# Optimization experiments

Measured on AMD Instinct MI355X. Metric: run time of the kernel, lower is better.

Reference implementation:

```python
import jax, jax.numpy as jnp
import numpy as np
from jax import lax

SCORE_THRESHOLD = 0.01
NMS_THRESHOLD = 0.5
MAX_DETECTIONS = 100
PRE_NMS_TOPK = 512  # fixed-shape candidate pool per class (tf NMS is unbounded; 512 >> max_detections covers it)
NEG_INF = -jnp.inf


def setup_inputs() -> dict:
    key = jax.random.key(0)
    k1, k2, k3, k4, k5 = jax.random.split(key, 5)
    B, N, C = 32, 50000, 10
    # valid (x1,y1,x2,y2) boxes: random top-left + positive width/height
    xy = jax.random.uniform(k1, (B, N, 2), dtype=jnp.float32) * 500.0
    wh = jax.random.uniform(k2, (B, N, 2), dtype=jnp.float32) * 100.0 + 1.0
    boxes = jnp.concatenate([xy, xy + wh], axis=-1)
    classification = jax.random.uniform(k3, (B, N, C), dtype=jnp.float32)
    rotation = jax.random.normal(k4, (B, N, 3), dtype=jnp.float32)
    translation = jax.random.normal(k5, (B, N, 3), dtype=jnp.float32)
    return {"boxes": boxes, "classification": classification,
            "rotation": rotation, "translation": translation}


def _iou_matrix(b):  # b: (K,4) in (x1,y1,x2,y2)
    x1, y1, x2, y2 = b[:, 0], b[:, 1], b[:, 2], b[:, 3]
    area = (x2 - x1) * (y2 - y1)  # (K,)
    ix1 = jnp.maximum(x1[:, None], x1[None, :])
    iy1 = jnp.maximum(y1[:, None], y1[None, :])
    ix2 = jnp.minimum(x2[:, None], x2[None, :])
    iy2 = jnp.minimum(y2[:, None], y2[None, :])
    inter = jnp.maximum(ix2 - ix1, 0.0) * jnp.maximum(iy2 - iy1, 0.0)
    union = area[:, None] + area[None, :] - inter
    return jnp.where(union > 0.0, inter / union, 0.0)  # (K,K)


def _greedy_nms_keep(iou, valid):
    # iou: (K,K) for boxes already sorted by descending score; valid: (K,) bool
    K = iou.shape[0]
    def body(suppressed, xs):
        iou_row, valid_i, i = xs
        keep_i = valid_i & jnp.logical_not(suppressed[i])
        suppressed = jnp.where(keep_i, suppressed | (iou_row > NMS_THRESHOLD), suppressed)
        return suppressed, keep_i
    _, keep = lax.scan(body, jnp.zeros((K,), bool), (iou, valid, jnp.arange(K)))
    return keep


def _per_class(scores, boxes_i):
    # scores: (N,), boxes_i: (N,4) -> kept candidate scores (K,) (-inf where dropped) and anchor idx (K,)
    sc = jnp.where(scores > SCORE_THRESHOLD, scores, NEG_INF)
    vals, idx = lax.top_k(sc, PRE_NMS_TOPK)          # sorted desc
    valid = vals > SCORE_THRESHOLD                    # also false for -inf pads
    iou = _iou_matrix(boxes_i[idx])
    keep = _greedy_nms_keep(iou, valid)
    keep = keep & (jnp.cumsum(keep.astype(jnp.int32)) <= MAX_DETECTIONS)
    return jnp.where(keep, vals, NEG_INF), idx


def _per_image(boxes_i, cls_i, rot_i, trans_i):
    # boxes_i (N,4), cls_i (N,C), rot_i (N,3), trans_i (N,3)
    C = cls_i.shape[1]
    sc_ck, idx_ck = jax.vmap(_per_class, in_axes=(1, None))(cls_i, boxes_i)  # (C,K)
    labels_ck = jnp.broadcast_to(jnp.arange(C, dtype=jnp.int32)[:, None], sc_ck.shape)
    sc_flat = sc_ck.reshape(-1)
    idx_flat = idx_ck.reshape(-1)
    lab_flat = labels_ck.reshape(-1)
    top_scores, sel = lax.top_k(sc_flat, MAX_DETECTIONS)   # global top-k across classes
    sel_idx = idx_flat[sel]
    sel_lab = lab_flat[sel]
    valid = jnp.isfinite(top_scores)
    out_boxes = jnp.where(valid[:, None], boxes_i[sel_idx], -1.0)
    out_scores = jnp.where(valid, top_scores, -1.0)
    out_labels = jnp.where(valid, sel_lab, -1).astype(jnp.int32)
    out_rot = jnp.where(valid[:, None], rot_i[sel_idx], -1.0)
    out_trans = jnp.where(valid[:, None], trans_i[sel_idx], -1.0)
    return out_boxes, out_scores, out_labels, out_rot, out_trans


def reference(boxes, classification, rotation, translation):
    return jax.vmap(_per_image)(boxes, classification, rotation, translation)
```

## Files before the change

kernel.cpp:

```cpp
#include <hip/hip_runtime.h>
#include <math.h>

typedef unsigned int u32;
typedef unsigned long long u64;

constexpr int NB   = 32;
constexpr int NN   = 50000;
constexpr int NC   = 10;
constexpr int KK   = 512;
constexpr int MAXD = 100;
constexpr int CAP  = 2048;
constexpr int LCAP = 192;
constexpr int GCH  = 2500;
constexpr int KMAX = 1024;
constexpr u32 TBIN = 252;

constexpr int OFF_BOX = 0;
constexpr int OFF_SC  = NB * MAXD * 4;
constexpr int OFF_LB  = OFF_SC + NB * MAXD;
constexpr int OFF_RT  = OFF_LB + NB * MAXD;
constexpr int OFF_TR  = OFF_RT + NB * MAXD * 3;

__device__ __forceinline__ u32 ord_f32(float s) {
  u32 u = __float_as_uint(s);
  return (u & 0x80000000u) ? ~u : (u | 0x80000000u);
}
__device__ __forceinline__ float unord_f32(u32 o) {
  u32 u = (o & 0x80000000u) ? (o & 0x7FFFFFFFu) : ~o;
  return __uint_as_float(u);
}
__device__ __forceinline__ u64 make_key(float s, u32 i) {
  float sp = (s > 0.01f) ? s : -INFINITY;
  return ((u64)ord_f32(sp) << 32) | (u64)(u32)(~i);
}
__device__ __forceinline__ u32 digest16(float x) {
  if (!(x > 0.01f)) return 0;
  u32 q = (u32)(x * 65536.0f);
  return q > 65535u ? 65535u : q;
}
__device__ __forceinline__ float readlane_f(float v, int lane) {
  return __int_as_float(__builtin_amdgcn_readlane(__float_as_int(v), lane));
}

__global__ __launch_bounds__(512) void gather_kernel(
    const float* __restrict__ cls, u64* __restrict__ glist,
    u32* __restrict__ gcnt) {
  const int blk = blockIdx.x;
  const int b = blk / 20, ch = blk % 20;
  const float* src = cls + (size_t)b * NN * NC + (size_t)ch * GCH * NC;
  __shared__ u32 lcnt[NC];
  __shared__ u32 lbase[NC];
  __shared__ u64 lbuf[NC][LCAP];
  const int t = threadIdx.x;
  if (t < NC) lcnt[t] = 0;
  __syncthreads();
  for (int q = t; q < GCH * NC / 4; q += 512) {
    float4 v = ((const float4*)src)[q];
    float arr[4] = {v.x, v.y, v.z, v.w};
#pragma unroll
    for (int k = 0; k < 4; ++k) {
      int e = q * 4 + k;
      int c = e % 10;
      float x = arr[k];
      if ((digest16(x) >> 8) >= TBIN) {
        u32 idx = (u32)((ch * (GCH * NC) + e) / 10);
        u32 p = atomicAdd(&lcnt[c], 1u);
        if (p < (u32)LCAP) {
          lbuf[c][p] = make_key(x, idx);
        } else {
          u32 g = atomicAdd(&gcnt[b * NC + c], 1u);
          if (g < (u32)CAP) glist[(size_t)(b * NC + c) * CAP + g] = make_key(x, idx);
        }
      }
    }
  }
  __syncthreads();
  if (t < NC) {
    u32 n = min(lcnt[t], (u32)LCAP);
    lbase[t] = atomicAdd(&gcnt[b * NC + t], n);
  }
  __syncthreads();
  for (int c = 0; c < NC; ++c) {
    u32 n = min(lcnt[c], (u32)LCAP);
    u32 base = lbase[c];
    for (u32 i = t; i < n; i += 512) {
      u32 p = base + i;
      if (p < (u32)CAP) glist[(size_t)(b * NC + c) * CAP + p] = lbuf[c][i];
    }
  }
}

__global__ __launch_bounds__(512) void repair_kernel(
    const float* __restrict__ cls, u64* __restrict__ glist,
    u32* __restrict__ gcnt) {
  const int bc = blockIdx.x;
  const u32 n0 = gcnt[bc];
  if (n0 >= (u32)KK && n0 <= (u32)KMAX) return;
  const int b = bc / NC, c = bc % NC;
  const float* sbase = cls + (size_t)b * NN * NC + c;
  __shared__ u32 hist[4096];
  __shared__ u32 s_d;
  const int t = threadIdx.x;
  for (int i = t; i < 4096; i += 512) hist[i] = 0;
  __syncthreads();
  for (int i = t; i < NN; i += 512)
    atomicAdd(&hist[digest16(sbase[(size_t)i * NC]) >> 4], 1u);
  __syncthreads();
  if (t == 0) {
    u32 run = 0, d = 1;
    for (int i = 4095; i >= 1; --i) {
      run += hist[i];
      if (run >= (u32)KK) { d = (u32)i; break; }
      d = 1;
    }
    s_d = d;
    gcnt[bc] = 0;
  }
  __syncthreads();
  const u32 dstar = s_d;
  for (int i = t; i < NN; i += 512) {
    float x = sbase[(size_t)i * NC];
    u32 dg = digest16(x) >> 4;
    if (dg >= dstar && dg >= 1) {
      u32 p = atomicAdd(&gcnt[bc], 1u);
      if (p < (u32)CAP) glist[(size_t)bc * CAP + p] = make_key(x, (u32)i);
    }
  }
}

__global__ __launch_bounds__(512) void selnms_kernel(
    const u64* __restrict__ glist, const u32* __restrict__ gcnt,
    const float* __restrict__ boxes, int* __restrict__ tidx,
    float* __restrict__ ksc) {
  const int bc = blockIdx.x;
  const int b = bc / NC;
  __shared__ __align__(16) u64 cand[KMAX];
  __shared__ __align__(16) ushort prank[KMAX][8];
  __shared__ u64 sel[KK];
  __shared__ float4 bx4[KK];
  __shared__ float ars[KK];
  __shared__ u64 kmask[8];
  const int t = threadIdx.x;
  const int lane = t & 63, wv = t >> 6;

  const int M = min((int)gcnt[bc], KMAX);
  for (int i = t; i < KMAX; i += 512)
    cand[i] = (i < M) ? glist[(size_t)bc * CAP + i] : (u64)i;
  sel[t] = make_key(-INFINITY, 0);
  __syncthreads();

  {
    u64 myk[16];
#pragma unroll
    for (int k = 0; k < 16; ++k) myk[k] = cand[lane + k * 64];
    int rnk[16];
#pragma unroll
    for (int k = 0; k < 16; ++k) rnk[k] = 0;
    const int j0 = wv * 128;
    for (int jj = 0; jj < 64; ++jj) {
      const ulonglong2 v = *(const ulonglong2*)&cand[j0 + jj * 2];
#pragma unroll
      for (int k = 0; k < 16; ++k) {
        rnk[k] += (v.x > myk[k]) ? 1 : 0;
        rnk[k] += (v.y > myk[k]) ? 1 : 0;
      }
    }
#pragma unroll
    for (int k = 0; k < 16; ++k) prank[lane + k * 64][wv] = (ushort)rnk[k];
  }
  __syncthreads();
#pragma unroll
  for (int h = 0; h < 2; ++h) {
    const int i = h * 512 + t;
    const uint4 pv = *(const uint4*)&prank[i][0];
    const int r = (int)(pv.x & 0xFFFFu) + (int)(pv.x >> 16) +
                  (int)(pv.y & 0xFFFFu) + (int)(pv.y >> 16) +
                  (int)(pv.z & 0xFFFFu) + (int)(pv.z >> 16) +
                  (int)(pv.w & 0xFFFFu) + (int)(pv.w >> 16);
    if (i < M && r < KK) sel[r] = cand[i];
  }
  __syncthreads();

  {
    const u64 k = sel[t];
    const int idx = (int)(~(u32)k);
    tidx[bc * KK + t] = idx;
    const float4 bx = *(const float4*)(boxes + ((size_t)b * NN + idx) * 4);
    bx4[t] = bx;
    ars[t] = (bx.z - bx.x) * (bx.w - bx.y);
  }
  __syncthreads();

  if (wv == 0) {
    float jx1[8], jy1[8], jx2[8], jy2[8], jar[8];
    u64 vw_[8], sup[8], kw[8];
#pragma unroll
    for (int q = 0; q < 8; ++q) {
      const int j = q * 64 + lane;
      float4 bb = bx4[j];
      jx1[q] = bb.x; jy1[q] = bb.y; jx2[q] = bb.z; jy2[q] = bb.w;
      jar[q] = ars[j];
      float sc = unord_f32((u32)(sel[j] >> 32));
      vw_[q] = __ballot(sc > 0.01f);
      sup[q] = 0;
      kw[q] = 0;
    }
    int count = 0;
    bool done = false;
#pragma unroll
    for (int w = 0; w < 8; ++w) {
      if (!done) {
        u64 av = vw_[w] & ~sup[w];
        while (av) {
          const int bbit = (int)__builtin_ctzll(av);
          kw[w] |= 1ull << bbit;
          if (++count == MAXD) { done = true; break; }
          const float bix1 = readlane_f(jx1[w], bbit);
          const float biy1 = readlane_f(jy1[w], bbit);
          const float bix2 = readlane_f(jx2[w], bbit);
          const float biy2 = readlane_f(jy2[w], bbit);
          const float bia  = readlane_f(jar[w], bbit);
#pragma unroll
          for (int q = 0; q < 8; ++q) {
            if (q >= w) {
              float ix1 = fmaxf(bix1, jx1[q]);
              float iy1 = fmaxf(biy1, jy1[q]);
              float ix2 = fminf(bix2, jx2[q]);
              float iy2 = fminf(biy2, jy2[q]);
              float iw = fmaxf(ix2 - ix1, 0.0f);
              float ih = fmaxf(iy2 - iy1, 0.0f);
              float inter = iw * ih;
              float uni = bia + jar[q] - inter;
              bool s = (uni > 0.0f) && ((inter - 0.5f * uni) > uni * 0x1p-25f);
              sup[q] |= __ballot(s);
            }
          }
          const u64 mask_gt = (bbit == 63) ? 0ull : (~0ull << (bbit + 1));
          av = vw_[w] & ~sup[w] & mask_gt;
        }
      }
    }
    if (lane < 8) {
      u64 word = kw[0];
#pragma unroll
      for (int q = 1; q < 8; ++q) word = (lane == q) ? kw[q] : word;
      kmask[lane] = word;
    }
  }
  __syncthreads();
  {
    const float sc = unord_f32((u32)(sel[t] >> 32));
    const bool keep = (kmask[t >> 6] >> (t & 63)) & 1ull;
    ksc[bc * KK + t] = keep ? sc : -INFINITY;
  }
}

__global__ __launch_bounds__(512) void final_kernel(
    const float* __restrict__ boxes, const float* __restrict__ rot,
    const float* __restrict__ trans, const int* __restrict__ tidx,
    const float* __restrict__ ksc, float* __restrict__ out) {
  const int b = blockIdx.x;
  __shared__ __align__(16) u64 ck[KMAX];
  __shared__ __align__(16) ushort prank[KMAX][8];
  __shared__ u64 top[MAXD];
  __shared__ int cnt;
  const int t = threadIdx.x;
  const int lane = t & 63, wv = t >> 6;
  if (t == 0) cnt = 0;
  if (t < MAXD) top[t] = make_key(-INFINITY, 0);
  for (int i = t; i < KMAX; i += 512) ck[i] = (u64)i;
  __syncthreads();
  for (int j = t; j < NC * KK; j += 512) {
    float s = ksc[b * NC * KK + j];
    if (s != -INFINITY) {
      int p = atomicAdd(&cnt, 1);
      if (p < KMAX) ck[p] = ((u64)ord_f32(s) << 32) | (u64)(u32)(~(u32)j);
    }
  }
  __syncthreads();
  const int n = min(cnt, KMAX);
  {
    u64 myk[16];
#pragma unroll
    for (int k = 0; k < 16; ++k) myk[k] = ck[lane + k * 64];
    int rnk[16];
#pragma unroll
    for (int k = 0; k < 16; ++k) rnk[k] = 0;
    const int j0 = wv * 128;
    for (int jj = 0; jj < 64; ++jj) {
      const ulonglong2 v = *(const ulonglong2*)&ck[j0 + jj * 2];
#pragma unroll
      for (int k = 0; k < 16; ++k) {
        rnk[k] += (v.x > myk[k]) ? 1 : 0;
        rnk[k] += (v.y > myk[k]) ? 1 : 0;
      }
    }
#pragma unroll
    for (int k = 0; k < 16; ++k) prank[lane + k * 64][wv] = (ushort)rnk[k];
  }
  __syncthreads();
#pragma unroll
  for (int h = 0; h < 2; ++h) {
    const int i = h * 512 + t;
    const uint4 pv = *(const uint4*)&prank[i][0];
    const int r = (int)(pv.x & 0xFFFFu) + (int)(pv.x >> 16) +
                  (int)(pv.y & 0xFFFFu) + (int)(pv.y >> 16) +
                  (int)(pv.z & 0xFFFFu) + (int)(pv.z >> 16) +
                  (int)(pv.w & 0xFFFFu) + (int)(pv.w >> 16);
    if (i < n && r < MAXD) top[r] = ck[i];
  }
  __syncthreads();

  if (t < MAXD) {
    float b0 = -1.f, b1 = -1.f, b2 = -1.f, b3 = -1.f;
    float os = -1.f, ol = -1.f;
    float r0 = -1.f, r1 = -1.f, r2 = -1.f;
    float t0 = -1.f, t1 = -1.f, t2 = -1.f;
    const u64 k = top[t];
    const float sc = unord_f32((u32)(k >> 32));
    if (sc != -INFINITY) {
      int j = (int)(~(u32)k);
      int c = j >> 9, slot = j & (KK - 1);
      int idx = tidx[(b * NC + c) * KK + slot];
      os = sc;
      ol = (float)c;
      const float4 bx = *(const float4*)(boxes + ((size_t)b * NN + idx) * 4);
      b0 = bx.x; b1 = bx.y; b2 = bx.z; b3 = bx.w;
      const float* rp = rot + ((size_t)b * NN + idx) * 3;
      r0 = rp[0]; r1 = rp[1]; r2 = rp[2];
      const float* tp = trans + ((size_t)b * NN + idx) * 3;
      t0 = tp[0]; t1 = tp[1]; t2 = tp[2];
    }
    const int o = b * MAXD + t;
    out[OFF_BOX + (size_t)o * 4 + 0] = b0;
    out[OFF_BOX + (size_t)o * 4 + 1] = b1;
    out[OFF_BOX + (size_t)o * 4 + 2] = b2;
    out[OFF_BOX + (size_t)o * 4 + 3] = b3;
    out[OFF_SC + o] = os;
    out[OFF_LB + o] = ol;
    out[OFF_RT + (size_t)o * 3 + 0] = r0;
    out[OFF_RT + (size_t)o * 3 + 1] = r1;
    out[OFF_RT + (size_t)o * 3 + 2] = r2;
    out[OFF_TR + (size_t)o * 3 + 0] = t0;
    out[OFF_TR + (size_t)o * 3 + 1] = t1;
    out[OFF_TR + (size_t)o * 3 + 2] = t2;
  }
}

extern "C" void kernel_launch(void* const* d_in, const int* in_sizes, int n_in,
                              void* d_out, int out_size, void* d_ws, size_t ws_size,
                              hipStream_t stream) {
  const float* boxes = (const float*)d_in[0];
  const float* cls   = (const float*)d_in[1];
  const float* rot   = (const float*)d_in[2];
  const float* trans = (const float*)d_in[3];
  float* out = (float*)d_out;

  u64* glist = (u64*)d_ws;
  int* tidx  = (int*)(glist + (size_t)NB * NC * CAP);
  float* ksc = (float*)(tidx + NB * NC * KK);
  u32* gcnt  = (u32*)(ksc + NB * NC * KK);

  hipMemsetAsync(gcnt, 0, NB * NC * sizeof(u32), stream);
  gather_kernel<<<NB * 20, 512, 0, stream>>>(cls, glist, gcnt);
  repair_kernel<<<NB * NC, 512, 0, stream>>>(cls, glist, gcnt);
  selnms_kernel<<<NB * NC, 512, 0, stream>>>(glist, gcnt, boxes, tidx, ksc);
  final_kernel<<<NB, 512, 0, stream>>>(boxes, rot, trans, tidx, ksc, out);
}
```

Before: 133.2 us.

## Split selection and NMS into separate kernels, one wavefront per class NMS

The fused select+NMS kernel is split in two. A selection kernel writes the sorted top-512 keys to global memory, and a new NMS kernel packs 8 (image,class) problems per block, one wavefront each. Before, a 512-thread block left 7 of its 8 wavefronts idle during the serial greedy NMS. This adds a kernel launch and a global round-trip of the 512 keys per class, and the NMS runs on only 40 blocks.

Result: slower. 150.6 us (+13.1%).

```diff
diff --git a/kernel.cpp b/kernel.cpp
--- a/kernel.cpp
+++ b/kernel.cpp
@@ -128,18 +128,13 @@
   }
 }
 
-__global__ __launch_bounds__(512) void selnms_kernel(
+__global__ __launch_bounds__(512) void sel_kernel(
     const u64* __restrict__ glist, const u32* __restrict__ gcnt,
-    const float* __restrict__ boxes, int* __restrict__ tidx,
-    float* __restrict__ ksc) {
+    u64* __restrict__ selg, int* __restrict__ tidx) {
   const int bc = blockIdx.x;
-  const int b = bc / NC;
   __shared__ __align__(16) u64 cand[KMAX];
   __shared__ __align__(16) ushort prank[KMAX][8];
   __shared__ u64 sel[KK];
-  __shared__ float4 bx4[KK];
-  __shared__ float ars[KK];
-  __shared__ u64 kmask[8];
   const int t = threadIdx.x;
   const int lane = t & 63, wv = t >> 6;
 
@@ -180,78 +175,79 @@
     if (i < M && r < KK) sel[r] = cand[i];
   }
   __syncthreads();
-
   {
     const u64 k = sel[t];
+    selg[(size_t)bc * KK + t] = k;
+    tidx[bc * KK + t] = (int)(~(u32)k);
+  }
+}
+
+__global__ __launch_bounds__(512) void nms_kernel(
+    const u64* __restrict__ selg, const int* __restrict__ tidx,
+    const float* __restrict__ boxes, float* __restrict__ ksc) {
+  const int lane = threadIdx.x & 63;
+  const int wv = threadIdx.x >> 6;
+  const int bc = blockIdx.x * 8 + wv;
+  const int b = bc / NC;
+
+  float jx1[8], jy1[8], jx2[8], jy2[8], jar[8], jsc[8];
+  u64 vw_[8], sup[8], kw[8];
+#pragma unroll
+  for (int q = 0; q < 8; ++q) {
+    const int j = q * 64 + lane;
+    const u64 k = selg[(size_t)bc * KK + j];
     const int idx = (int)(~(u32)k);
-    tidx[bc * KK + t] = idx;
     const float4 bx = *(const float4*)(boxes + ((size_t)b * NN + idx) * 4);
-    bx4[t] = bx;
-    ars[t] = (bx.z - bx.x) * (bx.w - bx.y);
-  }
-  __syncthreads();
-
-  if (wv == 0) {
-    float jx1[8], jy1[8], jx2[8], jy2[8], jar[8];
-    u64 vw_[8], sup[8], kw[8];
-#pragma unroll
-    for (int q = 0; q < 8; ++q) {
-      const int j = q * 64 + lane;
-      float4 bb = bx4[j];
-      jx1[q] = bb.x; jy1[q] = bb.y; jx2[q] = bb.z; jy2[q] = bb.w;
-      jar[q] = ars[j];
-      float sc = unord_f32((u32)(sel[j] >> 32));
-      vw_[q] = __ballot(sc > 0.01f);
-      sup[q] = 0;
-      kw[q] = 0;
-    }
-    int count = 0;
-    bool done = false;
-#pragma unroll
-    for (int w = 0; w < 8; ++w) {
-      if (!done) {
-        u64 av = vw_[w] & ~sup[w];
-        while (av) {
-          const int bbit = (int)__builtin_ctzll(av);
-          kw[w] |= 1ull << bbit;
-          if (++count == MAXD) { done = true; break; }
-          const float bix1 = readlane_f(jx1[w], bbit);
-          const float biy1 = readlane_f(jy1[w], bbit);
-          const float bix2 = readlane_f(jx2[w], bbit);
-          const float biy2 = readlane_f(jy2[w], bbit);
-          const float bia  = readlane_f(jar[w], bbit);
-#pragma unroll
-          for (int q = 0; q < 8; ++q) {
-            if (q >= w) {
-              float ix1 = fmaxf(bix1, jx1[q]);
-              float iy1 = fmaxf(biy1, jy1[q]);
-              float ix2 = fminf(bix2, jx2[q]);
-              float iy2 = fminf(biy2, jy2[q]);
-              float iw = fmaxf(ix2 - ix1, 0.0f);
-              float ih = fmaxf(iy2 - iy1, 0.0f);
-              float inter = iw * ih;
-              float uni = bia + jar[q] - inter;
-              bool s = (uni > 0.0f) && ((inter - 0.5f * uni) > uni * 0x1p-25f);
-              sup[q] |= __ballot(s);
-            }
+    jx1[q] = bx.x; jy1[q] = bx.y; jx2[q] = bx.z; jy2[q] = bx.w;
+    jar[q] = (bx.z - bx.x) * (bx.w - bx.y);
+    const float sc = unord_f32((u32)(k >> 32));
+    jsc[q] = sc;
+    vw_[q] = __ballot(sc > 0.01f);
+    sup[q] = 0;
+    kw[q] = 0;
+  }
+
+  int count = 0;
+  bool done = false;
+#pragma unroll
+  for (int w = 0; w < 8; ++w) {
+    if (!done) {
+      u64 av = vw_[w] & ~sup[w];
+      while (av) {
+        const int bbit = (int)__builtin_ctzll(av);
+        kw[w] |= 1ull << bbit;
+        if (++count == MAXD) { done = true; break; }
+        const float bix1 = readlane_f(jx1[w], bbit);
+        const float biy1 = readlane_f(jy1[w], bbit);
+        const float bix2 = readlane_f(jx2[w], bbit);
+        const float biy2 = readlane_f(jy2[w], bbit);
+        const float bia  = readlane_f(jar[w], bbit);
+#pragma unroll
+        for (int q = 0; q < 8; ++q) {
+          if (q >= w) {
+            float ix1 = fmaxf(bix1, jx1[q]);
+            float iy1 = fmaxf(biy1, jy1[q]);
+            float ix2 = fminf(bix2, jx2[q]);
+            float iy2 = fminf(biy2, jy2[q]);
+            float iw = fmaxf(ix2 - ix1, 0.0f);
+            float ih = fmaxf(iy2 - iy1, 0.0f);
+            float inter = iw * ih;
+            float uni = bia + jar[q] - inter;
+            bool s = (uni > 0.0f) && ((inter - 0.5f * uni) > uni * 0x1p-25f);
+            sup[q] |= __ballot(s);
           }
-          const u64 mask_gt = (bbit == 63) ? 0ull : (~0ull << (bbit + 1));
-          av = vw_[w] & ~sup[w] & mask_gt;
         }
+        const u64 mask_gt = (bbit == 63) ? 0ull : (~0ull << (bbit + 1));
+        av = vw_[w] & ~sup[w] & mask_gt;
       }
     }
-    if (lane < 8) {
-      u64 word = kw[0];
-#pragma unroll
-      for (int q = 1; q < 8; ++q) word = (lane == q) ? kw[q] : word;
-      kmask[lane] = word;
-    }
-  }
-  __syncthreads();
-  {
-    const float sc = unord_f32((u32)(sel[t] >> 32));
-    const bool keep = (kmask[t >> 6] >> (t & 63)) & 1ull;
-    ksc[bc * KK + t] = keep ? sc : -INFINITY;
+  }
+
+#pragma unroll
+  for (int q = 0; q < 8; ++q) {
+    const int j = q * 64 + lane;
+    const bool keep = (kw[q] >> lane) & 1ull;
+    ksc[(size_t)bc * KK + j] = keep ? jsc[q] : -INFINITY;
   }
 }
 
@@ -357,13 +353,15 @@
   float* out = (float*)d_out;
 
   u64* glist = (u64*)d_ws;
-  int* tidx  = (int*)(glist + (size_t)NB * NC * CAP);
+  u64* selg  = glist + (size_t)NB * NC * CAP;
+  int* tidx  = (int*)(selg + (size_t)NB * NC * KK);
   float* ksc = (float*)(tidx + NB * NC * KK);
   u32* gcnt  = (u32*)(ksc + NB * NC * KK);
 
   hipMemsetAsync(gcnt, 0, NB * NC * sizeof(u32), stream);
   gather_kernel<<<NB * 20, 512, 0, stream>>>(cls, glist, gcnt);
   repair_kernel<<<NB * NC, 512, 0, stream>>>(cls, glist, gcnt);
-  selnms_kernel<<<NB * NC, 512, 0, stream>>>(glist, gcnt, boxes, tidx, ksc);
+  sel_kernel<<<NB * NC, 512, 0, stream>>>(glist, gcnt, selg, tidx);
+  nms_kernel<<<40, 512, 0, stream>>>(selg, tidx, boxes, ksc);
   final_kernel<<<NB, 512, 0, stream>>>(boxes, rot, trans, tidx, ksc, out);
 }
```
